# Optimization experiments

Measured on AMD Instinct MI355X. Metric: run time of the kernel, lower is better.

## Reference

```python
import jax, jax.numpy as jnp
import numpy as np

NLAYERS = 8
NSUB = 4
L = NLAYERS * NSUB
DMIN, DMAX = 2.0, 20.0
SIGMOID_OFFSET = -1.0
H, W = 960, 1920
N_RAYS = 131072


def _grid_sample(img, grid):
    """torch.F.grid_sample equivalent: bilinear, align_corners=True, zeros padding.
    img: (B, C, H, W); grid: (B, Hg, Wg, 2) with grid[...,0]=x (width), grid[...,1]=y (height).
    Returns (B, C, Hg, Wg)."""
    B, C, Hh, Ww = img.shape
    x = (grid[..., 0] + 1.0) * 0.5 * (Ww - 1)
    y = (grid[..., 1] + 1.0) * 0.5 * (Hh - 1)
    x0 = jnp.floor(x)
    y0 = jnp.floor(y)
    x1 = x0 + 1.0
    y1 = y0 + 1.0
    wx1 = x - x0
    wy1 = y - y0
    bidx = jnp.arange(B)[:, None, None]

    def corner(iy, ix, w):
        valid = (ix >= 0) & (ix <= Ww - 1) & (iy >= 0) & (iy <= Hh - 1)
        iyc = jnp.clip(iy, 0, Hh - 1).astype(jnp.int32)
        ixc = jnp.clip(ix, 0, Ww - 1).astype(jnp.int32)
        v = img[bidx, :, iyc, ixc]  # (B, Hg, Wg, C)
        return jnp.where(valid[..., None], v, 0.0) * w[..., None]

    out = (corner(y0, x0, (1.0 - wy1) * (1.0 - wx1))
           + corner(y0, x1, (1.0 - wy1) * wx1)
           + corner(y1, x0, wy1 * (1.0 - wx1))
           + corner(y1, x1, wy1 * wx1))
    return jnp.moveaxis(out, -1, 1)


def setup_inputs() -> dict:
    key = jax.random.key(0)
    k1, k2, k3, k4 = jax.random.split(key, 4)
    origins = jax.random.uniform(k1, (N_RAYS, 3), jnp.float32)          # |O| < dmin -> valid intersections
    directions = jax.random.normal(k2, (N_RAYS, 3), jnp.float32)
    alpha = jax.random.uniform(k3, (L, 1, H, W), jnp.float32, -1.0, 1.0)
    rgb = jax.random.uniform(k4, (NLAYERS, 3, H, W), jnp.float32, -1.0, 1.0)
    pose = jnp.eye(4, dtype=jnp.float32)
    planes = jnp.asarray(1.0 / np.linspace(1.0 / DMIN, 1.0 / DMAX, L), jnp.float32)
    return {"origins": origins, "directions": directions, "pose": pose,
            "alpha": alpha, "rgb": rgb, "planes": planes}


def reference(origins, directions, pose, alpha, rgb, planes):
    center = pose[:3, 3]                                   # (3,)
    O = origins[:, None, :]                                # (N,1,3)
    D = directions[:, None, :]                             # (N,1,3)
    ray = O - center
    a = jnp.sum(D * D, axis=-1)                            # (N,1)
    b = 2.0 * jnp.sum(D * ray, axis=-1)                    # (N,1)
    c = jnp.sum(ray * ray, axis=-1) - planes[None, :] ** 2  # (N,L)
    disc = b * b - 4.0 * a * c
    sq = jnp.sqrt(disc)
    t0 = (-b + sq) / (2.0 * a)                             # (N,L)
    t1 = (-b - sq) / (2.0 * a)
    mask = (t0 * t1) < 0.0                                 # (N,L)
    inter = O + D * t0[:, :, None]                         # (N,L,3)

    xyz = inter - center
    xyzn = xyz / planes.reshape(1, -1, 1)                  # on unit sphere per layer
    uvs = jnp.stack([xyzn[..., 2],
                     jnp.arctan2(xyzn[..., 1], -xyzn[..., 0]) / jnp.pi], axis=2)  # (N,L,2)
    uvs = jnp.transpose(uvs, (1, 0, 2))[:, None]           # (L,1,N,2)

    alphas = _grid_sample(alpha, uvs)                      # (L,1,1,N)
    a_sig = jax.nn.sigmoid(alphas - SIGMOID_OFFSET)
    a_sig = jnp.transpose(a_sig, (0, 2, 3, 1))             # (L,1,N,1)
    m = jnp.transpose(mask, (1, 0))[:, None, :, None]      # (L,1,N,1)
    a_sig = jnp.where(m, a_sig, 0.0)

    rgbs = jax.nn.sigmoid(_grid_sample(rgb, uvs[::NSUB]))  # (nlayers,3,1,N)
    rgbs = jnp.transpose(rgbs, (0, 1, 3, 2))               # (nlayers,3,N,1)
    rgbs = jnp.repeat(rgbs, NSUB, axis=0)                  # (L,3,N,1)

    trans = jnp.cumprod(1.0 - a_sig, axis=0)
    excl = jnp.concatenate([jnp.ones_like(trans[:1]), trans[:-1]], axis=0)  # exclusive cumprod
    weight = excl * a_sig                                  # (L,1,N,1)
    out = jnp.sum(weight * rgbs, axis=0, keepdims=True)    # (1,3,N,1)
    return out
```

## Files before the change

kernel.cpp:

```cpp
#include <hip/hip_runtime.h>
#include <math.h>

namespace {
constexpr int kNRays = 131072;
constexpr int kNL = 8;
constexpr int kSub = 4;
constexpr int kH = 960;
constexpr int kW = 1920;
constexpr int kHW = kH * kW;

__device__ __forceinline__ float sigmoidf(float z) {
    return 1.0f / (1.0f + __expf(-z));
}

__device__ __forceinline__ void bilin_setup(float gx, float gy, int idx[4], float w[4]) {
    float x = (gx + 1.0f) * (0.5f * (float)(kW - 1));
    float y = (gy + 1.0f) * (0.5f * (float)(kH - 1));
    float x0f = floorf(x), y0f = floorf(y);
    float wx1 = x - x0f, wy1 = y - y0f;
    float wx0 = 1.0f - wx1, wy0 = 1.0f - wy1;
    bool vx0 = (x0f >= 0.0f) && (x0f <= (float)(kW - 1));
    bool vx1 = (x0f + 1.0f >= 0.0f) && (x0f + 1.0f <= (float)(kW - 1));
    bool vy0 = (y0f >= 0.0f) && (y0f <= (float)(kH - 1));
    bool vy1 = (y0f + 1.0f >= 0.0f) && (y0f + 1.0f <= (float)(kH - 1));
    int x0 = min(max((int)x0f, 0), kW - 1);
    int x1 = min(max((int)x0f + 1, 0), kW - 1);
    int y0 = min(max((int)y0f, 0), kH - 1);
    int y1 = min(max((int)y0f + 1, 0), kH - 1);
    idx[0] = y0 * kW + x0; w[0] = (vy0 && vx0) ? wy0 * wx0 : 0.0f;
    idx[1] = y0 * kW + x1; w[1] = (vy0 && vx1) ? wy0 * wx1 : 0.0f;
    idx[2] = y1 * kW + x0; w[2] = (vy1 && vx0) ? wy1 * wx0 : 0.0f;
    idx[3] = y1 * kW + x1; w[3] = (vy1 && vx1) ? wy1 * wx1 : 0.0f;
}
}

__global__ __launch_bounds__(256) void msi_field_kernel(
    const float* __restrict__ origins,
    const float* __restrict__ dirs,
    const float* __restrict__ pose,
    const float* __restrict__ alpha,
    const float* __restrict__ rgb,
    const float* __restrict__ planes,
    float* __restrict__ out)
{
    int i = blockIdx.x * blockDim.x + threadIdx.x;
    if (i >= kNRays) return;

    float cx = pose[3], cy = pose[7], cz = pose[11];
    float ox = origins[3*i+0], oy = origins[3*i+1], oz = origins[3*i+2];
    float dx = dirs[3*i+0],    dy = dirs[3*i+1],    dz = dirs[3*i+2];

    float rx = ox - cx, ry = oy - cy, rz = oz - cz;
    float a  = dx*dx + dy*dy + dz*dz;
    float b  = 2.0f * (dx*rx + dy*ry + dz*rz);
    float rr = rx*rx + ry*ry + rz*rz;
    float inv2a = 1.0f / (2.0f * a);

    float T = 1.0f;
    float accR = 0.0f, accG = 0.0f, accB = 0.0f;
    float sr = 0.0f, sg = 0.0f, sb = 0.0f;

    for (int nl = 0; nl < kNL; ++nl) {
        #pragma unroll
        for (int s = 0; s < kSub; ++s) {
            const int l = nl * kSub + s;
            float p = planes[l];
            float c = rr - p * p;
            float disc = b * b - 4.0f * a * c;
            float sq = sqrtf(disc);
            float t0 = (-b + sq) * inv2a;
            float t1 = (-b - sq) * inv2a;
            bool mask = (t0 * t1) < 0.0f;

            float hx = rx + dx * t0;
            float hy = ry + dy * t0;
            float hz = rz + dz * t0;
            float invp = 1.0f / p;
            float xn = hx * invp, yn = hy * invp, zn = hz * invp;

            float gx = zn;
            float gy = atan2f(yn, -xn) * 0.31830988618379067f;

            int idx[4]; float w[4];
            bilin_setup(gx, gy, idx, w);

            const float* aimg = alpha + (size_t)l * kHW;
            float av = w[0]*aimg[idx[0]] + w[1]*aimg[idx[1]]
                     + w[2]*aimg[idx[2]] + w[3]*aimg[idx[3]];
            float asig = mask ? sigmoidf(av + 1.0f) : 0.0f;

            if (s == 0) {
                const float* rimg = rgb + (size_t)nl * 3 * kHW;
                const float* gimg = rimg + kHW;
                const float* bimg = rimg + 2 * kHW;
                float rv = w[0]*rimg[idx[0]] + w[1]*rimg[idx[1]]
                         + w[2]*rimg[idx[2]] + w[3]*rimg[idx[3]];
                float gv = w[0]*gimg[idx[0]] + w[1]*gimg[idx[1]]
                         + w[2]*gimg[idx[2]] + w[3]*gimg[idx[3]];
                float bv = w[0]*bimg[idx[0]] + w[1]*bimg[idx[1]]
                         + w[2]*bimg[idx[2]] + w[3]*bimg[idx[3]];
                sr = sigmoidf(rv); sg = sigmoidf(gv); sb = sigmoidf(bv);
            }

            float wt = T * asig;
            accR += wt * sr;
            accG += wt * sg;
            accB += wt * sb;
            T *= (1.0f - asig);
        }
    }

    out[i]            = accR;
    out[kNRays + i]   = accG;
    out[2*kNRays + i] = accB;
}

extern "C" void kernel_launch(void* const* d_in, const int* in_sizes, int n_in,
                              void* d_out, int out_size, void* d_ws, size_t ws_size,
                              hipStream_t stream) {
    const float* origins = (const float*)d_in[0];
    const float* dirs    = (const float*)d_in[1];
    const float* pose    = (const float*)d_in[2];
    const float* alpha   = (const float*)d_in[3];
    const float* rgb     = (const float*)d_in[4];
    const float* planes  = (const float*)d_in[5];
    float* out = (float*)d_out;

    dim3 block(256);
    dim3 grid((kNRays + 255) / 256);
    hipLaunchKernelGGL(msi_field_kernel, grid, block, 0, stream,
                       origins, dirs, pose, alpha, rgb, planes, out);
}
```

Before: 532.5 us.

## Split each ray's layers across four lanes and combine with shuffle compositing

Each ray is now handled by four adjacent lanes, and each lane composites two of the eight layer groups. The partial (transmittance, colour) pairs are merged with an associative over-operator through two xor-shuffle steps, and lane 0 writes the result. The goal is more parallelism and more gathers in flight, which hides latency on a gather-bound kernel. The cost is four-fold redundant ray setup and a minimum-occupancy launch bound that may limit register use.

```diff
diff --git a/kernel.cpp b/kernel.cpp
--- a/kernel.cpp
+++ b/kernel.cpp
@@ -3,7 +3,8 @@
 
 namespace {
 constexpr int kNRays = 131072;
-constexpr int kNL = 8;
+constexpr int kLanesPerRay = 4;
+constexpr int kGroupsPerLane = 2;
 constexpr int kSub = 4;
 constexpr int kH = 960;
 constexpr int kW = 1920;
@@ -34,7 +35,7 @@
 }
 }
 
-__global__ __launch_bounds__(256) void msi_field_kernel(
+__global__ __launch_bounds__(256, 8) void msi_field_kernel(
     const float* __restrict__ origins,
     const float* __restrict__ dirs,
     const float* __restrict__ pose,
@@ -43,7 +44,9 @@
     const float* __restrict__ planes,
     float* __restrict__ out)
 {
-    int i = blockIdx.x * blockDim.x + threadIdx.x;
+    int tid = blockIdx.x * blockDim.x + threadIdx.x;
+    int i = tid / kLanesPerRay;
+    int r = tid & (kLanesPerRay - 1);
     if (i >= kNRays) return;
 
     float cx = pose[3], cy = pose[7], cz = pose[11];
@@ -60,7 +63,9 @@
     float accR = 0.0f, accG = 0.0f, accB = 0.0f;
     float sr = 0.0f, sg = 0.0f, sb = 0.0f;
 
-    for (int nl = 0; nl < kNL; ++nl) {
+    #pragma unroll
+    for (int g = 0; g < kGroupsPerLane; ++g) {
+        const int nl = r * kGroupsPerLane + g;
         #pragma unroll
         for (int s = 0; s < kSub; ++s) {
             const int l = nl * kSub + s;
@@ -110,9 +115,26 @@
         }
     }
 
-    out[i]            = accR;
-    out[kNRays + i]   = accG;
-    out[2*kNRays + i] = accB;
+    #pragma unroll
+    for (int m = 1; m <= 2; m <<= 1) {
+        float pT = __shfl_xor(T,    m);
+        float pR = __shfl_xor(accR, m);
+        float pG = __shfl_xor(accG, m);
+        float pB = __shfl_xor(accB, m);
+        if ((r & m) == 0) {
+            accR += T * pR; accG += T * pG; accB += T * pB;
+            T *= pT;
+        } else {
+            accR = pR + pT * accR; accG = pG + pT * accG; accB = pB + pT * accB;
+            T = pT * T;
+        }
+    }
+
+    if (r == 0) {
+        out[i]            = accR;
+        out[kNRays + i]   = accG;
+        out[2*kNRays + i] = accB;
+    }
 }
 
 extern "C" void kernel_launch(void* const* d_in, const int* in_sizes, int n_in,
@@ -126,8 +148,9 @@
     const float* planes  = (const float*)d_in[5];
     float* out = (float*)d_out;
 
+    const int total = kNRays * kLanesPerRay;
     dim3 block(256);
-    dim3 grid((kNRays + 255) / 256);
+    dim3 grid((total + 255) / 256);
     hipLaunchKernelGGL(msi_field_kernel, grid, block, 0, stream,
                        origins, dirs, pose, alpha, rgb, planes, out);
 }
```

After: 629.0 us. 18.1% more time.

## Sort rays by Morton-coded spherical UV bucket before texture sampling

Applied to the files above, without the earlier changes.

Adds a pre-pass that computes each ray's UV on a middle plane, quantizes it to a 64x64 grid with a Morton code, and builds a counting-sort permutation through a histogram, a single-block scan and an atomic scatter. The main kernel then processes rays in that permuted order, so neighbouring threads sample nearby texels. The goal is to cut the scattered, cache-unfriendly gathers from the large alpha and rgb images. In exchange it adds three small kernels, a memset, atomics, and non-coalesced reads of origins and directions plus scattered output writes in the main kernel.

```diff
diff --git a/kernel.cpp b/kernel.cpp
--- a/kernel.cpp
+++ b/kernel.cpp
@@ -8,9 +8,41 @@
 constexpr int kH = 960;
 constexpr int kW = 1920;
 constexpr int kHW = kH * kW;
+constexpr int kGridB = 64;
+constexpr int kNBuckets = kGridB * kGridB;
+constexpr int kKeyPlane = 20;
 
 __device__ __forceinline__ float sigmoidf(float z) {
     return 1.0f / (1.0f + __expf(-z));
+}
+
+__device__ __forceinline__ unsigned morton2(unsigned x, unsigned y) {
+    unsigned r = 0;
+    #pragma unroll
+    for (int i = 0; i < 6; ++i) {
+        r |= ((x >> i) & 1u) << (2 * i);
+        r |= ((y >> i) & 1u) << (2 * i + 1);
+    }
+    return r;
+}
+
+__device__ __forceinline__ void ray_uv(float rx, float ry, float rz,
+                                       float dx, float dy, float dz,
+                                       float p, float& gx, float& gy) {
+    float a  = dx*dx + dy*dy + dz*dz;
+    float b  = 2.0f * (dx*rx + dy*ry + dz*rz);
+    float rr = rx*rx + ry*ry + rz*rz;
+    float c = rr - p * p;
+    float disc = b * b - 4.0f * a * c;
+    float sq = sqrtf(fmaxf(disc, 0.0f));
+    float t0 = (-b + sq) / (2.0f * a);
+    float hx = rx + dx * t0;
+    float hy = ry + dy * t0;
+    float hz = rz + dz * t0;
+    float invp = 1.0f / p;
+    float xn = hx * invp, yn = hy * invp, zn = hz * invp;
+    gx = zn;
+    gy = atan2f(yn, -xn) * 0.31830988618379067f;
 }
 
 __device__ __forceinline__ void bilin_setup(float gx, float gy, int idx[4], float w[4]) {
@@ -34,6 +66,63 @@
 }
 }
 
+__global__ __launch_bounds__(256) void key_hist_kernel(
+    const float* __restrict__ origins, const float* __restrict__ dirs,
+    const float* __restrict__ pose, const float* __restrict__ planes,
+    unsigned* __restrict__ keys, unsigned* __restrict__ hist)
+{
+    int i = blockIdx.x * blockDim.x + threadIdx.x;
+    if (i >= kNRays) return;
+    float cx = pose[3], cy = pose[7], cz = pose[11];
+    float rx = origins[3*i+0] - cx, ry = origins[3*i+1] - cy, rz = origins[3*i+2] - cz;
+    float dx = dirs[3*i+0], dy = dirs[3*i+1], dz = dirs[3*i+2];
+    float gx, gy;
+    ray_uv(rx, ry, rz, dx, dy, dz, planes[kKeyPlane], gx, gy);
+    int qu = min(max((int)((gx * 0.5f + 0.5f) * (float)kGridB), 0), kGridB - 1);
+    int qv = min(max((int)((gy * 0.5f + 0.5f) * (float)kGridB), 0), kGridB - 1);
+    unsigned k = morton2((unsigned)qu, (unsigned)qv);
+    keys[i] = k;
+    atomicAdd(&hist[k], 1u);
+}
+
+__global__ __launch_bounds__(256) void scan_kernel(unsigned* __restrict__ hist)
+{
+    __shared__ unsigned part[256];
+    int t = threadIdx.x;
+    unsigned loc[kNBuckets / 256];
+    unsigned sum = 0;
+    #pragma unroll
+    for (int j = 0; j < kNBuckets / 256; ++j) {
+        loc[j] = hist[t * (kNBuckets / 256) + j];
+        sum += loc[j];
+    }
+    part[t] = sum;
+    __syncthreads();
+    for (int off = 1; off < 256; off <<= 1) {
+        unsigned v = (t >= off) ? part[t - off] : 0u;
+        __syncthreads();
+        part[t] += v;
+        __syncthreads();
+    }
+    unsigned prefix = part[t] - sum;
+    #pragma unroll
+    for (int j = 0; j < kNBuckets / 256; ++j) {
+        unsigned v = loc[j];
+        hist[t * (kNBuckets / 256) + j] = prefix;
+        prefix += v;
+    }
+}
+
+__global__ __launch_bounds__(256) void scatter_kernel(
+    const unsigned* __restrict__ keys, unsigned* __restrict__ offs,
+    unsigned* __restrict__ perm)
+{
+    int i = blockIdx.x * blockDim.x + threadIdx.x;
+    if (i >= kNRays) return;
+    unsigned pos = atomicAdd(&offs[keys[i]], 1u);
+    perm[pos] = (unsigned)i;
+}
+
 __global__ __launch_bounds__(256) void msi_field_kernel(
     const float* __restrict__ origins,
     const float* __restrict__ dirs,
@@ -41,10 +130,12 @@
     const float* __restrict__ alpha,
     const float* __restrict__ rgb,
     const float* __restrict__ planes,
+    const unsigned* __restrict__ perm,
     float* __restrict__ out)
 {
-    int i = blockIdx.x * blockDim.x + threadIdx.x;
-    if (i >= kNRays) return;
+    int slot = blockIdx.x * blockDim.x + threadIdx.x;
+    if (slot >= kNRays) return;
+    int i = (int)perm[slot];
 
     float cx = pose[3], cy = pose[7], cz = pose[11];
     float ox = origins[3*i+0], oy = origins[3*i+1], oz = origins[3*i+2];
@@ -126,8 +217,18 @@
     const float* planes  = (const float*)d_in[5];
     float* out = (float*)d_out;
 
+    unsigned* hist = (unsigned*)d_ws;
+    unsigned* keys = hist + kNBuckets;
+    unsigned* perm = keys + kNRays;
+
+    hipMemsetAsync(hist, 0, kNBuckets * sizeof(unsigned), stream);
+
     dim3 block(256);
-    dim3 grid((kNRays + 255) / 256);
-    hipLaunchKernelGGL(msi_field_kernel, grid, block, 0, stream,
-                       origins, dirs, pose, alpha, rgb, planes, out);
-}
+    dim3 gridR((kNRays + 255) / 256);
+    hipLaunchKernelGGL(key_hist_kernel, gridR, block, 0, stream,
+                       origins, dirs, pose, planes, keys, hist);
+    hipLaunchKernelGGL(scan_kernel, dim3(1), block, 0, stream, hist);
+    hipLaunchKernelGGL(scatter_kernel, gridR, block, 0, stream, keys, hist, perm);
+    hipLaunchKernelGGL(msi_field_kernel, gridR, block, 0, stream,
+                       origins, dirs, pose, alpha, rgb, planes, perm, out);
+}
```

New measurement: 495.5 us. 7.0% less time.
